# Kernel optimization log

Measured on AMD Instinct MI355X. Metric: run time of the kernel, lower is better.

## Reference

```python
import jax, jax.numpy as jnp
import numpy as np

N, E, D = 50000, 800000, 256

def setup_inputs() -> dict:
    key = jax.random.key(0)
    ks = jax.random.split(key, 12)
    s = 1.0 / np.sqrt(D)
    return {
        "x": jax.random.normal(ks[0], (N, D), dtype=jnp.float32),
        "src": jax.random.randint(ks[1], (E,), 0, N, dtype=jnp.int64),
        "dst": jax.random.randint(ks[2], (E,), 0, N, dtype=jnp.int64),
        "W_w": jax.random.normal(ks[3], (D, D), dtype=jnp.float32) * s,
        "W_b": jnp.zeros((D,), dtype=jnp.float32),
        "U_w": jax.random.normal(ks[4], (D, D), dtype=jnp.float32) * s,
        "U_b": jnp.zeros((D,), dtype=jnp.float32),
        "V_w": jax.random.normal(ks[5], (D, D), dtype=jnp.float32) * s,
        "V_b": jnp.zeros((D,), dtype=jnp.float32),
        "attn_l": jax.random.normal(ks[6], (D,), dtype=jnp.float32) * s,
        "attn_r": jax.random.normal(ks[7], (D,), dtype=jnp.float32) * s,
        "gamma": jnp.ones((D,), dtype=jnp.float32),
        "beta": jnp.zeros((D,), dtype=jnp.float32),
    }

def reference(x, src, dst, W_w, W_b, U_w, U_b, V_w, V_b, attn_l, attn_r, gamma, beta):
    # node transforms (dropout p=0 -> identity)
    Wh = x @ W_w + W_b            # [N, D]
    Uh = x @ U_w + U_b            # [N, D]
    Vh = x @ V_w + V_b            # [N, D]
    out_src = Wh * attn_l         # [N, D]
    out_dst = Wh * attn_r         # [N, D]
    # per-edge gate: sigma = sigmoid(out_src[u] + out_dst[v])  [E, D]
    sigma = jax.nn.sigmoid(out_src[src] + out_dst[dst])
    # aggregate to destination nodes
    sum_sigma_h = jax.ops.segment_sum(Vh[src] * sigma, dst, num_segments=N)
    sum_sigma = jax.ops.segment_sum(sigma, dst, num_segments=N)
    h = Uh + sum_sigma_h / (sum_sigma + 1e-6)
    # layer norm (eps=1e-6, affine)
    mu = jnp.mean(h, axis=-1, keepdims=True)
    var = jnp.mean((h - mu) ** 2, axis=-1, keepdims=True)
    h = (h - mu) / jnp.sqrt(var + 1e-6) * gamma + beta
    h = jax.nn.relu(h)
    return x + h  # residual
```

## Files before the change

### kernel.cpp

```cpp
#include <hip/hip_runtime.h>
#include <hip/hip_bf16.h>

#define NN 50000
#define NE 800000
#define NB 196
#define NROWPAD 50048

#define XCVT_BLOCKS 6250
#define TW_BLOCKS   192
#define HIST_BLOCKS 3125

typedef __attribute__((ext_vector_type(8))) short short8;
typedef __attribute__((ext_vector_type(4))) float floatx4;
typedef unsigned short u16;
typedef unsigned int u32;

__device__ __forceinline__ u16 f2bf(float f) {
    u32 u = __float_as_uint(f);
    u += 0x7FFFu + ((u >> 16) & 1u);
    return (u16)(u >> 16);
}
__device__ __forceinline__ float bf_lo(u32 u) { return __uint_as_float(u << 16); }
__device__ __forceinline__ float bf_hi(u32 u) { return __uint_as_float(u & 0xFFFF0000u); }
__device__ __forceinline__ u32 pack_bf(float lo, float hi) {
    return (u32)f2bf(lo) | ((u32)f2bf(hi) << 16);
}
__device__ __forceinline__ void gl_lds16(const void* g, void* l) {
    __builtin_amdgcn_global_load_lds((const __attribute__((address_space(1))) void*)g,
                                     (__attribute__((address_space(3))) void*)l, 16, 0, 0);
}

#if __has_builtin(__builtin_amdgcn_exp2f)
#define EXP2F(x) __builtin_amdgcn_exp2f(x)
#else
#define EXP2F(x) exp2f(x)
#endif

__global__ __launch_bounds__(256) void prep_kernel(
    const float* __restrict__ x, u16* __restrict__ xbf,
    const float* __restrict__ W, const float* __restrict__ U, const float* __restrict__ V,
    u16* __restrict__ wT, const int* __restrict__ dst, int* __restrict__ deg, int do_xcvt) {
    __shared__ float s[32][33];
    int b = blockIdx.x;
    int xb = do_xcvt ? XCVT_BLOCKS : 0;
    if (b < xb) {
        size_t i = ((size_t)b * 256 + threadIdx.x) * 8;
        floatx4 f0 = *(const floatx4*)(x + i);
        floatx4 f1 = *(const floatx4*)(x + i + 4);
        uint4 pk;
        pk.x = pack_bf(f0[0], f0[1]);
        pk.y = pack_bf(f0[2], f0[3]);
        pk.z = pack_bf(f1[0], f1[1]);
        pk.w = pack_bf(f1[2], f1[3]);
        *(uint4*)(xbf + i) = pk;
    } else if (b < xb + TW_BLOCKS) {
        int bb = b - xb;
        int g = bb >> 6, rem = bb & 63;
        int r0 = (rem & 7) * 32, c0 = (rem >> 3) * 32;
        const float* M = (g == 0) ? W : ((g == 1) ? U : V);
        int tx = threadIdx.x & 31, ty = threadIdx.x >> 5;
#pragma unroll
        for (int k = 0; k < 4; ++k)
            s[ty + k * 8][tx] = M[(size_t)(r0 + ty + k * 8) * 256 + c0 + tx];
        __syncthreads();
#pragma unroll
        for (int k = 0; k < 4; ++k)
            wT[(size_t)(g * 256 + c0 + ty + k * 8) * 256 + r0 + tx] = f2bf(s[tx][ty + k * 8]);
    } else {
        int e = (b - xb - TW_BLOCKS) * 256 + threadIdx.x;
        if (e < NE) atomicAdd(&deg[dst[e]], 1);
    }
}

__global__ __launch_bounds__(256) void scanA_kernel(const int* __restrict__ deg, int* __restrict__ bsum) {
    int t = threadIdx.x;
    int i = blockIdx.x * 256 + t;
    int v = (i < NN) ? deg[i] : 0;
#pragma unroll
    for (int m = 32; m; m >>= 1) v += __shfl_xor(v, m, 64);
    __shared__ int ws[4];
    if ((t & 63) == 0) ws[t >> 6] = v;
    __syncthreads();
    if (t == 0) bsum[blockIdx.x] = ws[0] + ws[1] + ws[2] + ws[3];
}

__global__ __launch_bounds__(256) void scanB_kernel(const int* __restrict__ bsum, int* __restrict__ bpre,
                                                    int* __restrict__ rows_end) {
    int t = threadIdx.x, lane = t & 63, wv = t >> 6;
    int v = (t < NB) ? bsum[t] : 0;
    int inc = v;
#pragma unroll
    for (int off = 1; off < 64; off <<= 1) {
        int u = __shfl_up(inc, off, 64);
        if (lane >= off) inc += u;
    }
    __shared__ int wsum[4];
    if (lane == 63) wsum[wv] = inc;
    __syncthreads();
    int woff = 0;
    for (int k = 0; k < wv; ++k) woff += wsum[k];
    if (t < NB) bpre[t] = woff + inc - v;
    if (t == 255) rows_end[0] = woff + inc;
}

__global__ __launch_bounds__(256) void scanC_kernel(const int* __restrict__ deg, const int* __restrict__ bpre,
                                                    int* __restrict__ rows, int* __restrict__ cursor) {
    int t = threadIdx.x, lane = t & 63, wv = t >> 6;
    int i = blockIdx.x * 256 + t;
    int v = (i < NN) ? deg[i] : 0;
    int inc = v;
#pragma unroll
    for (int off = 1; off < 64; off <<= 1) {
        int u = __shfl_up(inc, off, 64);
        if (lane >= off) inc += u;
    }
    __shared__ int wsum[4];
    if (lane == 63) wsum[wv] = inc;
    __syncthreads();
    int woff = bpre[blockIdx.x];
    for (int k = 0; k < wv; ++k) woff += wsum[k];
    int excl = woff + inc - v;
    if (i < NN) { rows[i] = excl; cursor[i] = excl; }
}

__global__ void scatter_kernel(const int* __restrict__ src, const int* __restrict__ dst,
                               int* __restrict__ cursor, int* __restrict__ esrc) {
    int e = blockIdx.x * 256 + threadIdx.x;
    if (e < NE) {
        int d = dst[e];
        int pos = atomicAdd(&cursor[d], 1);
        esrc[pos] = src[e];
    }
}

template<bool USE_BF>
__global__ __launch_bounds__(256, 2) void gemm2_kernel(
    const u16* __restrict__ xbf, const float* __restrict__ xf, const u16* __restrict__ wT,
    const float* __restrict__ Wb, const float* __restrict__ Ub, const float* __restrict__ Vb,
    u16* __restrict__ WVh, float* __restrict__ Uh) {
    __shared__ __align__(16) u16 Bs[128 * 256];

    int rb = blockIdx.x * 128;
    int cgy = blockIdx.y;
    int cbg = cgy * 128;
    int t = threadIdx.x, lane = t & 63, w = t >> 6;

    int arow = rb + w * 32 + (lane & 15);
    short8 afr[2][8];
    if (USE_BF) {
#pragma unroll
        for (int rg = 0; rg < 2; ++rg)
#pragma unroll
            for (int ks = 0; ks < 8; ++ks)
                afr[rg][ks] = *(const short8*)(xbf + (size_t)(arow + rg * 16) * 256 + ks * 32 + (lane >> 4) * 8);
    } else {
#pragma unroll
        for (int rg = 0; rg < 2; ++rg)
#pragma unroll
            for (int ks = 0; ks < 8; ++ks) {
                int row = arow + rg * 16;
                const float* p = xf + ((size_t)(row < NN ? row : 0)) * 256 + ks * 32 + (lane >> 4) * 8;
                floatx4 f0 = *(const floatx4*)(p);
                floatx4 f1 = *(const floatx4*)(p + 4);
                uint4 pk;
                pk.x = pack_bf(f0[0], f0[1]);
                pk.y = pack_bf(f0[2], f0[3]);
                pk.z = pack_bf(f1[0], f1[1]);
                pk.w = pack_bf(f1[2], f1[3]);
                afr[rg][ks] = *(short8*)&pk;
            }
    }

#pragma unroll
    for (int i = 0; i < 16; ++i) {
        int ci = (w * 16 + i) * 2 + (lane >> 5);
        int q = (lane & 31) ^ (ci & 7);
        gl_lds16(wT + (size_t)(cbg + ci) * 256 + q * 8, Bs + (w * 16 + i) * 512);
    }
    __syncthreads();

    floatx4 acc[2][8] = {};
#pragma unroll
    for (int ks = 0; ks < 8; ++ks) {
#pragma unroll
        for (int cf = 0; cf < 8; ++cf) {
            int ci = cf * 16 + (lane & 15);
            int q = (ks * 4 + (lane >> 4)) ^ (ci & 7);
            short8 bfrag = *(const short8*)(Bs + ci * 256 + q * 8);
            acc[0][cf] = __builtin_amdgcn_mfma_f32_16x16x32_bf16(afr[0][ks], bfrag, acc[0][cf], 0, 0, 0);
            acc[1][cf] = __builtin_amdgcn_mfma_f32_16x16x32_bf16(afr[1][ks], bfrag, acc[1][cf], 0, 0, 0);
        }
    }

    int g = cbg >> 8;
    int cloc = cbg & 255;
    const float* bias = (g == 0) ? Wb : ((g == 1) ? Ub : Vb);

    __syncthreads();

    if (g == 1) {
        float* Ct = (float*)Bs;
#pragma unroll
        for (int rg = 0; rg < 2; ++rg)
#pragma unroll
            for (int cf = 0; cf < 8; ++cf) {
                int col = cf * 16 + (lane & 15);
                float bv = bias[cloc + col];
#pragma unroll
                for (int r = 0; r < 4; ++r) {
                    int rl = w * 32 + rg * 16 + (lane >> 4) * 4 + r;
                    Ct[rl * 128 + col] = acc[rg][cf][r] + bv;
                }
            }
        __syncthreads();
        int row = t >> 1, half = t & 1;
        int grow = rb + row;
        if (grow < NN) {
            const uint4* srcp = (const uint4*)(Ct + row * 128 + half * 64);
            float* dstp = Uh + (size_t)grow * 256 + cloc + half * 64;
#pragma unroll
            for (int k = 0; k < 16; ++k)
                *(uint4*)(dstp + k * 4) = srcp[k];
        }
    } else {
        u16* Ct = (u16*)Bs;
#pragma unroll
        for (int rg = 0; rg < 2; ++rg)
#pragma unroll
            for (int cf = 0; cf < 8; ++cf) {
                int col = cf * 16 + (lane & 15);
                float bv = bias[cloc + col];
#pragma unroll
                for (int r = 0; r < 4; ++r) {
                    int rl = w * 32 + rg * 16 + (lane >> 4) * 4 + r;
                    Ct[rl * 128 + col] = f2bf(acc[rg][cf][r] + bv);
                }
            }
        __syncthreads();
        int row = t >> 1, half = t & 1;
        int grow = rb + row;
        if (grow < NN) {
            const uint4* srcp = (const uint4*)(Ct + row * 128 + half * 64);
            u16* dstp = WVh + (size_t)grow * 512 + (g == 2 ? 256 : 0) + cloc + half * 64;
#pragma unroll
            for (int k = 0; k < 8; ++k)
                *(uint4*)(dstp + k * 8) = srcp[k];
        }
    }
}

__global__ __launch_bounds__(256) void node_kernel(
    const u16* __restrict__ WVh, const float* __restrict__ x,
    const int* __restrict__ rows, const int* __restrict__ esrc,
    const float* __restrict__ attn_l, const float* __restrict__ attn_r,
    const float* __restrict__ gamma, const float* __restrict__ beta,
    float* inout) {
    int wv = threadIdx.x >> 6, lane = threadIdx.x & 63;
    int v = blockIdx.x * 4 + wv;
    if (v >= NN) return;
    int c0 = lane * 4;

    const float NL2E = -1.44269504f;
    floatx4 alv = *(const floatx4*)(attn_l + c0);
    floatx4 arv = *(const floatx4*)(attn_r + c0);
    uint2 wvv = *(const uint2*)(WVh + (size_t)v * 512 + c0);
    float al2[4] = { alv[0] * NL2E, alv[1] * NL2E, alv[2] * NL2E, alv[3] * NL2E };
    float td2[4] = { bf_lo(wvv.x) * arv[0] * NL2E, bf_hi(wvv.x) * arv[1] * NL2E,
                     bf_lo(wvv.y) * arv[2] * NL2E, bf_hi(wvv.y) * arv[3] * NL2E };

    float acc_h[4] = {0.f, 0.f, 0.f, 0.f};
    float acc_s[4] = {0.f, 0.f, 0.f, 0.f};

    auto edge = [&](uint2 wu, uint2 vu) {
        float wf[4] = { bf_lo(wu.x), bf_hi(wu.x), bf_lo(wu.y), bf_hi(wu.y) };
        float vf[4] = { bf_lo(vu.x), bf_hi(vu.x), bf_lo(vu.y), bf_hi(vu.y) };
#pragma unroll
        for (int j = 0; j < 4; ++j) {
            float m = fmaf(wf[j], al2[j], td2[j]);
            float s = __builtin_amdgcn_rcpf(1.0f + EXP2F(m));
            acc_s[j] += s;
            acc_h[j] = fmaf(s, vf[j], acc_h[j]);
        }
    };

    int e = rows[v], e1 = rows[v + 1];
    for (; e + 8 <= e1; e += 8) {
        int us[8];
#pragma unroll
        for (int q = 0; q < 8; ++q) us[q] = esrc[e + q];
        uint2 wu[8], vu[8];
#pragma unroll
        for (int q = 0; q < 8; ++q) {
            const u16* p = WVh + (size_t)us[q] * 512 + c0;
            wu[q] = *(const uint2*)p;
            vu[q] = *(const uint2*)(p + 256);
        }
#pragma unroll
        for (int q = 0; q < 8; ++q) edge(wu[q], vu[q]);
    }
    for (; e + 2 <= e1; e += 2) {
        int ua = esrc[e], ub = esrc[e + 1];
        const u16* pa = WVh + (size_t)ua * 512 + c0;
        const u16* pb = WVh + (size_t)ub * 512 + c0;
        uint2 wa = *(const uint2*)pa, va = *(const uint2*)(pa + 256);
        uint2 wb = *(const uint2*)pb, vb = *(const uint2*)(pb + 256);
        edge(wa, va); edge(wb, vb);
    }
    for (; e < e1; ++e) {
        int u = esrc[e];
        const u16* p = WVh + (size_t)u * 512 + c0;
        uint2 wu = *(const uint2*)p, vu = *(const uint2*)(p + 256);
        edge(wu, vu);
    }

    floatx4 uh = *(const floatx4*)(inout + (size_t)v * 256 + c0);
    float h[4];
#pragma unroll
    for (int j = 0; j < 4; ++j)
        h[j] = uh[j] + acc_h[j] * __builtin_amdgcn_rcpf(acc_s[j] + 1e-6f);

    float s01 = h[0] + h[1] + h[2] + h[3];
#pragma unroll
    for (int m = 32; m; m >>= 1) s01 += __shfl_xor(s01, m, 64);
    float mu = s01 * (1.0f / 256.0f);
    float d[4] = { h[0] - mu, h[1] - mu, h[2] - mu, h[3] - mu };
    float sq = d[0] * d[0] + d[1] * d[1] + d[2] * d[2] + d[3] * d[3];
#pragma unroll
    for (int m = 32; m; m >>= 1) sq += __shfl_xor(sq, m, 64);
    float inv = rsqrtf(sq * (1.0f / 256.0f) + 1e-6f);

    floatx4 gm = *(const floatx4*)(gamma + c0);
    floatx4 bt = *(const floatx4*)(beta + c0);
    floatx4 xr = *(const floatx4*)(x + (size_t)v * 256 + c0);
    floatx4 res;
#pragma unroll
    for (int j = 0; j < 4; ++j) {
        float y = d[j] * inv * gm[j] + bt[j];
        y = fmaxf(y, 0.0f);
        res[j] = xr[j] + y;
    }
    *(floatx4*)(inout + (size_t)v * 256 + c0) = res;
}

extern "C" void kernel_launch(void* const* d_in, const int* in_sizes, int n_in,
                              void* d_out, int out_size, void* d_ws, size_t ws_size,
                              hipStream_t stream) {
    const float* x       = (const float*)d_in[0];
    const int*   src     = (const int*)d_in[1];
    const int*   dst     = (const int*)d_in[2];
    const float* W_w     = (const float*)d_in[3];
    const float* W_b     = (const float*)d_in[4];
    const float* U_w     = (const float*)d_in[5];
    const float* U_b     = (const float*)d_in[6];
    const float* V_w     = (const float*)d_in[7];
    const float* V_b     = (const float*)d_in[8];
    const float* attn_l  = (const float*)d_in[9];
    const float* attn_r  = (const float*)d_in[10];
    const float* gamma   = (const float*)d_in[11];
    const float* beta    = (const float*)d_in[12];

    char* ws = (char*)d_ws;
    size_t off = 0;
    auto alloc = [&](size_t bytes) -> char* {
        char* p = ws + off;
        off += (bytes + 255) & ~(size_t)255;
        return p;
    };
    u16* WVh     = (u16*)alloc((size_t)NN * 512 * 2);
    u16* wT      = (u16*)alloc((size_t)768 * 256 * 2);
    int* deg     = (int*)alloc((size_t)NN * 4);
    int* rows    = (int*)alloc((size_t)(NN + 1) * 4);
    int* cursor  = (int*)alloc((size_t)NN * 4);
    int* esrc    = (int*)alloc((size_t)NE * 4);
    int* bsum    = (int*)alloc((size_t)NB * 4);
    int* bpre    = (int*)alloc((size_t)NB * 4);
    u16* xbf     = (u16*)alloc((size_t)NROWPAD * 256 * 2);
    bool use_bf  = (ws_size >= off);

    float* Uh_f32 = (float*)d_out;

    hipMemsetAsync(deg, 0, (size_t)NN * 4, stream);

    int xb = use_bf ? XCVT_BLOCKS : 0;
    prep_kernel<<<xb + TW_BLOCKS + HIST_BLOCKS, 256, 0, stream>>>(
        x, xbf, W_w, U_w, V_w, wT, dst, deg, use_bf ? 1 : 0);

    scanA_kernel<<<NB, 256, 0, stream>>>(deg, bsum);
    scanB_kernel<<<1, 256, 0, stream>>>(bsum, bpre, rows + NN);
    scanC_kernel<<<NB, 256, 0, stream>>>(deg, bpre, rows, cursor);
    scatter_kernel<<<(NE + 255) / 256, 256, 0, stream>>>(src, dst, cursor, esrc);

    dim3 gg((NN + 127) / 128, 6);
    if (use_bf) {
        gemm2_kernel<true><<<gg, 256, 0, stream>>>(xbf, x, wT, W_b, U_b, V_b, WVh, Uh_f32);
    } else {
        gemm2_kernel<false><<<gg, 256, 0, stream>>>(nullptr, x, wT, W_b, U_b, V_b, WVh, Uh_f32);
    }

    node_kernel<<<(NN + 3) / 4, 256, 0, stream>>>(
        WVh, x, rows, esrc, attn_l, attn_r, gamma, beta, (float*)d_out);
}
```

Baseline: 303.0 us.

## Drop LDS staging of B in GEMM, remap workgroups per XCD, split node kernel

The GEMM now reads the B (weight) fragments straight from global memory instead of staging them into LDS through global_load_lds, which removes a block-wide barrier and frees most of the LDS. The epilogue uses a small per-wave swizzled LDS buffer, synchronised with s_waitcnt instead of __syncthreads. The 2D grid becomes a 1D grid whose block IDs are remapped so that consecutive tiles sharing the same A rows land on the same XCD, which is meant to improve L2 reuse. The node kernel is launched twice over the two halves of the node range, which adds a launch but has no obvious benefit; the uncached B reads may also raise L1/L2 traffic.

```diff
diff --git a/kernel.cpp b/kernel.cpp
--- a/kernel.cpp
+++ b/kernel.cpp
@@ -9,6 +9,7 @@
 #define XCVT_BLOCKS 6250
 #define TW_BLOCKS   192
 #define HIST_BLOCKS 3125
+#define GEMM_NWG    2346
 
 typedef __attribute__((ext_vector_type(8))) short short8;
 typedef __attribute__((ext_vector_type(4))) float floatx4;
@@ -24,10 +25,6 @@
 __device__ __forceinline__ float bf_hi(u32 u) { return __uint_as_float(u & 0xFFFF0000u); }
 __device__ __forceinline__ u32 pack_bf(float lo, float hi) {
     return (u32)f2bf(lo) | ((u32)f2bf(hi) << 16);
-}
-__device__ __forceinline__ void gl_lds16(const void* g, void* l) {
-    __builtin_amdgcn_global_load_lds((const __attribute__((address_space(1))) void*)g,
-                                     (__attribute__((address_space(3))) void*)l, 16, 0, 0);
 }
 
 #if __has_builtin(__builtin_amdgcn_exp2f)
@@ -134,15 +131,19 @@
 }
 
 template<bool USE_BF>
-__global__ __launch_bounds__(256, 2) void gemm2_kernel(
+__global__ __launch_bounds__(256, 2) void gemm3_kernel(
     const u16* __restrict__ xbf, const float* __restrict__ xf, const u16* __restrict__ wT,
     const float* __restrict__ Wb, const float* __restrict__ Ub, const float* __restrict__ Vb,
     u16* __restrict__ WVh, float* __restrict__ Uh) {
-    __shared__ __align__(16) u16 Bs[128 * 256];
-
-    int rb = blockIdx.x * 128;
-    int cgy = blockIdx.y;
+    __shared__ __align__(16) char Cs[4][8192];
+
+    int orig = blockIdx.x;
+    int xcd = orig & 7, j = orig >> 3;
+    int wgid = (xcd < 2 ? xcd * 294 : 2 * 294 + (xcd - 2) * 293) + j;
+    int rb = (wgid / 6) * 128;
+    int cgy = wgid % 6;
     int cbg = cgy * 128;
+
     int t = threadIdx.x, lane = t & 63, w = t >> 6;
 
     int arow = rb + w * 32 + (lane & 15);
@@ -171,22 +172,13 @@
             }
     }
 
-#pragma unroll
-    for (int i = 0; i < 16; ++i) {
-        int ci = (w * 16 + i) * 2 + (lane >> 5);
-        int q = (lane & 31) ^ (ci & 7);
-        gl_lds16(wT + (size_t)(cbg + ci) * 256 + q * 8, Bs + (w * 16 + i) * 512);
-    }
-    __syncthreads();
-
+    const u16* wTb = wT + (size_t)(cbg + (lane & 15)) * 256 + (lane >> 4) * 8;
     floatx4 acc[2][8] = {};
 #pragma unroll
     for (int ks = 0; ks < 8; ++ks) {
 #pragma unroll
         for (int cf = 0; cf < 8; ++cf) {
-            int ci = cf * 16 + (lane & 15);
-            int q = (ks * 4 + (lane >> 4)) ^ (ci & 7);
-            short8 bfrag = *(const short8*)(Bs + ci * 256 + q * 8);
+            short8 bfrag = *(const short8*)(wTb + (size_t)cf * 16 * 256 + ks * 32);
             acc[0][cf] = __builtin_amdgcn_mfma_f32_16x16x32_bf16(afr[0][ks], bfrag, acc[0][cf], 0, 0, 0);
             acc[1][cf] = __builtin_amdgcn_mfma_f32_16x16x32_bf16(afr[1][ks], bfrag, acc[1][cf], 0, 0, 0);
         }
@@ -196,55 +188,59 @@
     int cloc = cbg & 255;
     const float* bias = (g == 0) ? Wb : ((g == 1) ? Ub : Vb);
 
-    __syncthreads();
-
     if (g == 1) {
-        float* Ct = (float*)Bs;
-#pragma unroll
-        for (int rg = 0; rg < 2; ++rg)
+        float* Ct = (float*)&Cs[w][0];
+#pragma unroll
+        for (int rg = 0; rg < 2; ++rg) {
 #pragma unroll
             for (int cf = 0; cf < 8; ++cf) {
                 int col = cf * 16 + (lane & 15);
                 float bv = bias[cloc + col];
+                int q = col >> 2;
 #pragma unroll
                 for (int r = 0; r < 4; ++r) {
-                    int rl = w * 32 + rg * 16 + (lane >> 4) * 4 + r;
-                    Ct[rl * 128 + col] = acc[rg][cf][r] + bv;
+                    int rr = (lane >> 4) * 4 + r;
+                    Ct[rr * 128 + ((q ^ (rr & 7)) << 2) + (col & 3)] = acc[rg][cf][r] + bv;
                 }
             }
-        __syncthreads();
-        int row = t >> 1, half = t & 1;
-        int grow = rb + row;
-        if (grow < NN) {
-            const uint4* srcp = (const uint4*)(Ct + row * 128 + half * 64);
-            float* dstp = Uh + (size_t)grow * 256 + cloc + half * 64;
-#pragma unroll
-            for (int k = 0; k < 16; ++k)
-                *(uint4*)(dstp + k * 4) = srcp[k];
+            asm volatile("s_waitcnt lgkmcnt(0)" ::: "memory");
+            int row = lane >> 2, qc = lane & 3;
+            int grow = rb + w * 32 + rg * 16 + row;
+            if (grow < NN) {
+                float* dstp = Uh + (size_t)grow * 256 + cloc + qc * 32;
+#pragma unroll
+                for (int k2 = 0; k2 < 8; ++k2) {
+                    int pq = (qc * 8 + k2) ^ (row & 7);
+                    *(floatx4*)(dstp + k2 * 4) = *(const floatx4*)(Ct + row * 128 + pq * 4);
+                }
+            }
+            asm volatile("s_waitcnt lgkmcnt(0)" ::: "memory");
         }
     } else {
-        u16* Ct = (u16*)Bs;
+        u16* Ct = (u16*)&Cs[w][0];
 #pragma unroll
         for (int rg = 0; rg < 2; ++rg)
 #pragma unroll
             for (int cf = 0; cf < 8; ++cf) {
                 int col = cf * 16 + (lane & 15);
                 float bv = bias[cloc + col];
+                int q = col >> 3;
 #pragma unroll
                 for (int r = 0; r < 4; ++r) {
-                    int rl = w * 32 + rg * 16 + (lane >> 4) * 4 + r;
-                    Ct[rl * 128 + col] = f2bf(acc[rg][cf][r] + bv);
+                    int rr = rg * 16 + (lane >> 4) * 4 + r;
+                    Ct[rr * 128 + ((q ^ (rr & 7)) << 3) + (col & 7)] = f2bf(acc[rg][cf][r] + bv);
                 }
             }
-        __syncthreads();
-        int row = t >> 1, half = t & 1;
-        int grow = rb + row;
+        asm volatile("s_waitcnt lgkmcnt(0)" ::: "memory");
+        int row = lane >> 1, half = lane & 1;
+        int grow = rb + w * 32 + row;
         if (grow < NN) {
-            const uint4* srcp = (const uint4*)(Ct + row * 128 + half * 64);
             u16* dstp = WVh + (size_t)grow * 512 + (g == 2 ? 256 : 0) + cloc + half * 64;
 #pragma unroll
-            for (int k = 0; k < 8; ++k)
-                *(uint4*)(dstp + k * 8) = srcp[k];
+            for (int k2 = 0; k2 < 8; ++k2) {
+                int pq = (half * 8 + k2) ^ (row & 7);
+                *(uint4*)(dstp + k2 * 8) = *(const uint4*)(Ct + row * 128 + pq * 8);
+            }
         }
     }
 }
@@ -254,10 +250,10 @@
     const int* __restrict__ rows, const int* __restrict__ esrc,
     const float* __restrict__ attn_l, const float* __restrict__ attn_r,
     const float* __restrict__ gamma, const float* __restrict__ beta,
-    float* inout) {
+    float* inout, int vbase, int vend) {
     int wv = threadIdx.x >> 6, lane = threadIdx.x & 63;
-    int v = blockIdx.x * 4 + wv;
-    if (v >= NN) return;
+    int v = vbase + blockIdx.x * 4 + wv;
+    if (v >= vend) return;
     int c0 = lane * 4;
 
     const float NL2E = -1.44269504f;
@@ -390,13 +386,14 @@
     scanC_kernel<<<NB, 256, 0, stream>>>(deg, bpre, rows, cursor);
     scatter_kernel<<<(NE + 255) / 256, 256, 0, stream>>>(src, dst, cursor, esrc);
 
-    dim3 gg((NN + 127) / 128, 6);
     if (use_bf) {
-        gemm2_kernel<true><<<gg, 256, 0, stream>>>(xbf, x, wT, W_b, U_b, V_b, WVh, Uh_f32);
+        gemm3_kernel<true><<<GEMM_NWG, 256, 0, stream>>>(xbf, x, wT, W_b, U_b, V_b, WVh, Uh_f32);
     } else {
-        gemm2_kernel<false><<<gg, 256, 0, stream>>>(nullptr, x, wT, W_b, U_b, V_b, WVh, Uh_f32);
-    }
-
-    node_kernel<<<(NN + 3) / 4, 256, 0, stream>>>(
-        WVh, x, rows, esrc, attn_l, attn_r, gamma, beta, (float*)d_out);
-}
+        gemm3_kernel<false><<<GEMM_NWG, 256, 0, stream>>>(nullptr, x, wT, W_b, U_b, V_b, WVh, Uh_f32);
+    }
+
+    node_kernel<<<6250, 256, 0, stream>>>(
+        WVh, x, rows, esrc, attn_l, attn_r, gamma, beta, (float*)d_out, 0, 25000);
+    node_kernel<<<6250, 256, 0, stream>>>(
+        WVh, x, rows, esrc, attn_l, attn_r, gamma, beta, (float*)d_out, 25000, NN);
+}
```

Result: slower. 352.3 us (+16.3%).
